# Kernel optimization log

Measured on AMD Instinct MI355X. Metric: run time of the kernel, lower is better.

## Reference

```python
import jax, jax.numpy as jnp
import numpy as np

BN_EPS = 1e-5
L2_EPS = 1e-12


def _normalize_adj(adj):
    # faithful to normalize_adj_torch: D^{-1/2} scaling applied as
    # (adj @ diag(r)).T @ diag(r)  ==  adj.T * r[:,None] * r[None,:]
    rowsum = adj.sum(1)
    r = jnp.power(rowsum, -0.5)
    r = jnp.where(jnp.isinf(r), 0.0, r)
    return adj.T * r[:, None] * r[None, :]


def _graph_conv(x, adj_n, W, b):
    # y = adj @ x (+ self), y @ W + b, then L2-normalize over feature dim
    y = jnp.einsum('ij,bjd->bid', adj_n, x) + x
    y = jnp.einsum('bnd,de->bne', y, W) + b
    norm = jnp.linalg.norm(y, axis=2, keepdims=True)
    return y / jnp.maximum(norm, L2_EPS)


def _batch_norm_nodes(x):
    # BatchNorm1d(num_features = N) in training mode with fresh params:
    # normalize over (batch, feature) dims per node channel, biased variance
    mean = x.mean(axis=(0, 2), keepdims=True)
    var = x.var(axis=(0, 2), keepdims=True)
    return (x - mean) / jnp.sqrt(var + BN_EPS)


def setup_inputs() -> dict:
    key = jax.random.key(0)
    ks = jax.random.split(key, 5)
    B, N, D = 4, 8192, 64
    H, E, C = 128, 256, 16
    x = jax.random.normal(ks[0], (B, N, D), dtype=jnp.float32)
    adj = jax.random.uniform(ks[1], (N, N), dtype=jnp.float32)
    W1 = jax.random.normal(ks[2], (D, H), dtype=jnp.float32) * 0.1
    b1 = jnp.zeros((H,), dtype=jnp.float32)
    W2 = jax.random.normal(ks[3], (H, E), dtype=jnp.float32) * 0.1
    b2 = jnp.zeros((E,), dtype=jnp.float32)
    Wp = jax.random.normal(ks[4], (E, C), dtype=jnp.float32) * 0.1
    bp = jnp.zeros((C,), dtype=jnp.float32)
    return {"x": x, "adj": adj, "W1": W1, "b1": b1, "W2": W2,
            "b2": b2, "Wp": Wp, "bp": bp}


def reference(x, adj, W1, b1, W2, b2, Wp, bp):
    adj_n = _normalize_adj(adj)
    g1 = _graph_conv(x, adj_n, W1, b1)
    g1 = jax.nn.relu(g1)
    g1 = _batch_norm_nodes(g1)
    g1 = _graph_conv(g1, adj_n, W2, b2)
    g1 = jax.nn.relu(g1)
    g1 = _batch_norm_nodes(g1)
    pred = jnp.einsum('bne,ec->bnc', g1, Wp) + bp
    # Softmax over dim=1 (node axis), as in the original
    return jax.nn.softmax(pred, axis=1)
```

## Files before the change

### kernel.cpp

```cpp
#include <hip/hip_runtime.h>
#include <hip/hip_bf16.h>
#include <cstdint>
#include <cstddef>

typedef unsigned short u16;
typedef __attribute__((ext_vector_type(8))) short bf16x8;
typedef __attribute__((ext_vector_type(4))) float f32x4;
typedef __attribute__((ext_vector_type(4))) unsigned short u16x4;

#define B_ 4
#define N_ 8192
#define D_ 64
#define H_ 128
#define E_ 256
#define C_ 16

__device__ __forceinline__ u16 f2bf(float f) {
  unsigned u = __builtin_bit_cast(unsigned, f);
  u += 0x7fffu + ((u >> 16) & 1u);
  return (u16)(u >> 16);
}
__device__ __forceinline__ float bf2f(u16 u) {
  return __builtin_bit_cast(float, ((unsigned)u) << 16);
}

__device__ __forceinline__ float wave_sum(float v) {
  v += __shfl_xor(v, 32, 64); v += __shfl_xor(v, 16, 64); v += __shfl_xor(v, 8, 64);
  v += __shfl_xor(v, 4, 64);  v += __shfl_xor(v, 2, 64);  v += __shfl_xor(v, 1, 64);
  return v;
}
__device__ __forceinline__ float wave_max(float v) {
  v = fmaxf(v, __shfl_xor(v, 32, 64)); v = fmaxf(v, __shfl_xor(v, 16, 64));
  v = fmaxf(v, __shfl_xor(v, 8, 64));  v = fmaxf(v, __shfl_xor(v, 4, 64));
  v = fmaxf(v, __shfl_xor(v, 2, 64));  v = fmaxf(v, __shfl_xor(v, 1, 64));
  return v;
}

__device__ __forceinline__ void gld16(const void* g, void* l) {
  __builtin_amdgcn_global_load_lds((const __attribute__((address_space(1))) void*)g,
                                   (__attribute__((address_space(3))) void*)l, 16, 0, 0);
}

__global__ __launch_bounds__(256) void k_zero(float* __restrict__ p, int n) {
  int i = blockIdx.x * 256 + threadIdx.x;
  if (i < n) p[i] = 0.f;
}

__global__ __launch_bounds__(256) void k_transpose(const float* __restrict__ adj, u16* __restrict__ adjT,
                                                   float* __restrict__ rsum) {
  __shared__ float tile[64][65];
  int bi = blockIdx.x & 127, bj = blockIdx.x >> 7;
  int i0 = bi * 64, j0 = bj * 64;
  int t = threadIdx.x;
#pragma unroll
  for (int q = 0; q < 4; ++q) {
    int idx = q * 256 + t; int jl = idx >> 4, c4 = idx & 15;
    float4 v = *(const float4*)(adj + (size_t)(j0 + jl) * N_ + i0 + c4 * 4);
    tile[jl][c4 * 4 + 0] = v.x; tile[jl][c4 * 4 + 1] = v.y;
    tile[jl][c4 * 4 + 2] = v.z; tile[jl][c4 * 4 + 3] = v.w;
    float s = (v.x + v.y) + (v.z + v.w);
    s += __shfl_xor(s, 1, 64); s += __shfl_xor(s, 2, 64);
    s += __shfl_xor(s, 4, 64); s += __shfl_xor(s, 8, 64);
    if ((t & 15) == 0) atomicAdd(&rsum[j0 + jl], s);
  }
  __syncthreads();
#pragma unroll
  for (int q = 0; q < 4; ++q) {
    int idx = q * 256 + t; int il = idx >> 4, c4 = idx & 15;
    u16x4 o;
    o.x = f2bf(tile[c4 * 4 + 0][il]); o.y = f2bf(tile[c4 * 4 + 1][il]);
    o.z = f2bf(tile[c4 * 4 + 2][il]); o.w = f2bf(tile[c4 * 4 + 3][il]);
    *(u16x4*)(adjT + (size_t)(i0 + il) * N_ + j0 + c4 * 4) = o;
  }
}

__global__ __launch_bounds__(256) void k_rsqrt(const float* __restrict__ rsum, float* __restrict__ rr) {
  int i = blockIdx.x * 256 + threadIdx.x;
  float s = rsum[i];
  rr[i] = s > 0.f ? rsqrtf(s) : 0.f;
}

__global__ __launch_bounds__(256) void k_xt(const float* __restrict__ x, const float* __restrict__ rr,
                                            u16* __restrict__ xt) {
  __shared__ float tile[64][65];
  int b = blockIdx.x >> 7, j0 = (blockIdx.x & 127) * 64;
  int t = threadIdx.x;
#pragma unroll
  for (int q = 0; q < 4; ++q) {
    int idx = q * 256 + t; int jl = idx >> 4, c4 = idx & 15;
    float4 v = *(const float4*)(x + ((size_t)b * N_ + j0 + jl) * D_ + c4 * 4);
    float rv = rr[j0 + jl];
    tile[jl][c4 * 4 + 0] = v.x * rv; tile[jl][c4 * 4 + 1] = v.y * rv;
    tile[jl][c4 * 4 + 2] = v.z * rv; tile[jl][c4 * 4 + 3] = v.w * rv;
  }
  __syncthreads();
#pragma unroll
  for (int q = 0; q < 4; ++q) {
    int idx = q * 256 + t; int dl = idx >> 4, c4 = idx & 15;
    u16x4 o;
    o.x = f2bf(tile[c4 * 4 + 0][dl]); o.y = f2bf(tile[c4 * 4 + 1][dl]);
    o.z = f2bf(tile[c4 * 4 + 2][dl]); o.w = f2bf(tile[c4 * 4 + 3][dl]);
    *(u16x4*)(xt + (size_t)(b * 64 + dl) * N_ + j0 + c4 * 4) = o;
  }
}

template<int BM, int BN, int KS>
__global__ __launch_bounds__(256) void k_gemm(const u16* __restrict__ A, const u16* __restrict__ B,
                                              u16* __restrict__ Cp, int N) {
  constexpr int BK = 32;
  __shared__ __align__(16) u16 As[BM * BK];
  __shared__ __align__(16) u16 Bs[BN * BK];
  const int tid = threadIdx.x;
  const int nb = N / BN;
  const int bn = blockIdx.x % nb;
  const int kb = (blockIdx.x / nb) % KS;
  const int bm = blockIdx.x / (nb * KS);
  const int m0 = bm * BM, n0 = bn * BN;
  const int kbeg = kb * (N_ / KS), kend = kbeg + N_ / KS;
  constexpr int WM = BM / 2, WN = BN / 2;
  constexpr int FM = WM / 16, FN = WN / 16;
  const int wave = tid >> 6, lane = tid & 63;
  const int wm = (wave >> 1) * WM, wn = (wave & 1) * WN;
  const int lr = lane & 15, lk = lane >> 4;

  f32x4 acc[FM][FN];
#pragma unroll
  for (int a = 0; a < FM; ++a)
#pragma unroll
    for (int b = 0; b < FN; ++b) acc[a][b] = (f32x4){0.f, 0.f, 0.f, 0.f};

  for (int k0 = kbeg; k0 < kend; k0 += BK) {
#pragma unroll
    for (int it = 0; it < BM / 64; ++it) {
      int c = it * 256 + tid;
      gld16(A + (size_t)(m0 + (c >> 2)) * N_ + k0 + (c & 3) * 8,
            As + ((size_t)it * 256 + (tid & 192)) * 8);
    }
#pragma unroll
    for (int it = 0; it < BN / 64; ++it) {
      int c = it * 256 + tid;
      gld16(B + (size_t)(n0 + (c >> 2)) * N_ + k0 + (c & 3) * 8,
            Bs + ((size_t)it * 256 + (tid & 192)) * 8);
    }
    __syncthreads();
    bf16x8 av[FM], bv[FN];
#pragma unroll
    for (int f = 0; f < FM; ++f)
      av[f] = *(const bf16x8*)(As + (wm + f * 16 + lr) * BK + lk * 8);
#pragma unroll
    for (int f = 0; f < FN; ++f)
      bv[f] = *(const bf16x8*)(Bs + (wn + f * 16 + lr) * BK + lk * 8);
#pragma unroll
    for (int fm = 0; fm < FM; ++fm)
#pragma unroll
      for (int fn = 0; fn < FN; ++fn)
        acc[fm][fn] = __builtin_amdgcn_mfma_f32_16x16x32_bf16(av[fm], bv[fn], acc[fm][fn], 0, 0, 0);
    __syncthreads();
  }
  u16* Cs = Cp + (size_t)kb * N_ * N;
#pragma unroll
  for (int fm = 0; fm < FM; ++fm) {
    int row0 = m0 + wm + fm * 16 + lk * 4;
#pragma unroll
    for (int fn = 0; fn < FN; ++fn) {
      int col = n0 + wn + fn * 16 + lr;
#pragma unroll
      for (int p = 0; p < 4; ++p)
        Cs[(size_t)(row0 + p) * N + col] = f2bf(acc[fm][fn][p]);
    }
  }
}

__global__ __launch_bounds__(256) void k_epi1(const u16* __restrict__ T1p, const float* __restrict__ x,
    const float* __restrict__ rr, const float* __restrict__ W1, const float* __restrict__ b1,
    float* __restrict__ g1n, u16* __restrict__ g1t) {
  union SharedU { float ys[16][256]; u16 gb[512][18]; };
  __shared__ SharedU su;
  __shared__ float zbuf[16][512];
  __shared__ float rs[16];
  const int t = threadIdx.x;
  const int i0 = blockIdx.x * 16;
  constexpr size_t SL = (size_t)N_ * 256;
  if (t < 16) rs[t] = rr[i0 + t];
  __syncthreads();
#pragma unroll
  for (int q = 0; q < 16; ++q) {
    int idx = q * 256 + t; int n = idx >> 8, c = idx & 255, b = c >> 6, d = c & 63;
    size_t ti = (size_t)(i0 + n) * 256 + c;
    float s = bf2f(T1p[ti]) + bf2f(T1p[ti + SL]) + bf2f(T1p[ti + 2 * SL]) + bf2f(T1p[ti + 3 * SL]);
    su.ys[n][c] = rs[n] * s + x[((size_t)b * N_ + i0 + n) * D_ + d];
  }
  const int h = t & 127, bh = t >> 7;
  float w[64];
#pragma unroll
  for (int d = 0; d < 64; ++d) w[d] = W1[d * H_ + h];
  float b1h = b1[h];
  __syncthreads();
  for (int n = 0; n < 16; ++n) {
    float za = b1h, zb = b1h;
#pragma unroll
    for (int d = 0; d < 64; ++d) {
      za += su.ys[n][bh * 64 + d] * w[d];
      zb += su.ys[n][(bh + 2) * 64 + d] * w[d];
    }
    zbuf[n][bh * 128 + h] = za;
    zbuf[n][(bh + 2) * 128 + h] = zb;
  }
  __syncthreads();
  const int wv = t >> 6, lane = t & 63;
#pragma unroll
  for (int nn = 0; nn < 4; ++nn) {
    int n = wv * 4 + nn;
    float v[8], nb2[8];
#pragma unroll
    for (int q = 0; q < 8; ++q) { v[q] = zbuf[n][q * 64 + lane]; }
#pragma unroll
    for (int q = 0; q < 8; ++q) nb2[q] = wave_sum(v[q] * v[q]);
    float inv0 = 1.f / fmaxf(sqrtf(nb2[0] + nb2[1]), 1e-12f);
    float inv1 = 1.f / fmaxf(sqrtf(nb2[2] + nb2[3]), 1e-12f);
    float inv2 = 1.f / fmaxf(sqrtf(nb2[4] + nb2[5]), 1e-12f);
    float inv3 = 1.f / fmaxf(sqrtf(nb2[6] + nb2[7]), 1e-12f);
    float sc[4] = {inv0, inv1, inv2, inv3};
    float t1 = 0.f, t2 = 0.f;
#pragma unroll
    for (int q = 0; q < 8; ++q) {
      v[q] = fmaxf(v[q] * sc[q >> 1], 0.f);
      t1 += v[q]; t2 += v[q] * v[q];
    }
    float s1 = wave_sum(t1), s2 = wave_sum(t2);
    float m = s1 * (1.f / 512.f);
    float var = s2 * (1.f / 512.f) - m * m;
    float iv = rsqrtf(var + 1e-5f);
    float rv = rs[n];
#pragma unroll
    for (int q = 0; q < 8; ++q) {
      float g = (v[q] - m) * iv;
      g1n[(size_t)(i0 + n) * 512 + q * 64 + lane] = g;
      su.gb[q * 64 + lane][n] = f2bf(g * rv);
    }
  }
  __syncthreads();
#pragma unroll
  for (int rep = 0; rep < 2; ++rep) {
    int c = rep * 256 + t;
    const unsigned* src = (const unsigned*)&su.gb[c][0];
    uint4 o0, o1;
    o0.x = src[0]; o0.y = src[1]; o0.z = src[2]; o0.w = src[3];
    o1.x = src[4]; o1.y = src[5]; o1.z = src[6]; o1.w = src[7];
    uint4* dst = (uint4*)(g1t + (size_t)c * N_ + i0);
    dst[0] = o0; dst[1] = o1;
  }
}

__global__ __launch_bounds__(256) void k_epi2(const u16* __restrict__ T2p, const float* __restrict__ g1n,
    const float* __restrict__ rr, const float* __restrict__ W2, const float* __restrict__ b2,
    float* __restrict__ g2n) {
  __shared__ __align__(16) float ysm[8 * 512];
  __shared__ __align__(16) float W2s[32 * 256];
  __shared__ float red1[128];
  __shared__ float nv[32];
  __shared__ float redA[32], redB[32];
  __shared__ float mn[8], iv[8];
  constexpr size_t SL = (size_t)N_ * 512;
  int i0 = blockIdx.x * 8, t = threadIdx.x;
#pragma unroll
  for (int q = 0; q < 4; ++q) {
    int idx = q * 256 + t; int n = idx >> 7, c4 = idx & 127;
    int i = i0 + n;
    float rv = rr[i];
    size_t ti = (size_t)i * 512 + c4 * 4;
    u16x4 p0 = *(const u16x4*)(T2p + ti);
    u16x4 p1 = *(const u16x4*)(T2p + SL + ti);
    float4 g = *(const float4*)(g1n + ti);
    float4 y;
    y.x = rv * (bf2f(p0.x) + bf2f(p1.x)) + g.x;
    y.y = rv * (bf2f(p0.y) + bf2f(p1.y)) + g.y;
    y.z = rv * (bf2f(p0.z) + bf2f(p1.z)) + g.z;
    y.w = rv * (bf2f(p0.w) + bf2f(p1.w)) + g.w;
    *(float4*)&ysm[n * 512 + c4 * 4] = y;
  }
  int e = t;
  float z[8][4];
#pragma unroll
  for (int n = 0; n < 8; ++n)
#pragma unroll
    for (int b = 0; b < 4; ++b) z[n][b] = 0.f;

  for (int hc = 0; hc < H_; hc += 32) {
    __syncthreads();
#pragma unroll
    for (int q = 0; q < 8; ++q) {
      int idx = q * 256 + t;
      ((float4*)W2s)[idx] = ((const float4*)(W2 + (size_t)hc * 256))[idx];
    }
    __syncthreads();
#pragma unroll
    for (int h4 = 0; h4 < 32; h4 += 4) {
      float w0 = W2s[(h4 + 0) * 256 + e];
      float w1 = W2s[(h4 + 1) * 256 + e];
      float w2 = W2s[(h4 + 2) * 256 + e];
      float w3 = W2s[(h4 + 3) * 256 + e];
#pragma unroll
      for (int n = 0; n < 8; ++n) {
#pragma unroll
        for (int b = 0; b < 4; ++b) {
          float4 y = *(const float4*)&ysm[n * 512 + b * 128 + hc + h4];
          z[n][b] += y.x * w0 + y.y * w1 + y.z * w2 + y.w * w3;
        }
      }
    }
  }
  float b2e = b2[e];
  int wave = t >> 6, lane = t & 63;
#pragma unroll
  for (int n = 0; n < 8; ++n)
#pragma unroll
    for (int b = 0; b < 4; ++b) {
      z[n][b] += b2e;
      float s = wave_sum(z[n][b] * z[n][b]);
      if (lane == 0) red1[n * 16 + b * 4 + wave] = s;
    }
  __syncthreads();
  if (t < 32) {
    float s = red1[t * 4 + 0] + red1[t * 4 + 1] + red1[t * 4 + 2] + red1[t * 4 + 3];
    nv[t] = fmaxf(sqrtf(s), 1e-12f);
  }
  __syncthreads();
#pragma unroll
  for (int n = 0; n < 8; ++n) {
    float s1 = 0.f, s2 = 0.f;
#pragma unroll
    for (int b = 0; b < 4; ++b) {
      z[n][b] = fmaxf(z[n][b] / nv[n * 4 + b], 0.f);
      s1 += z[n][b]; s2 += z[n][b] * z[n][b];
    }
    s1 = wave_sum(s1); s2 = wave_sum(s2);
    if (lane == 0) { redA[n * 4 + wave] = s1; redB[n * 4 + wave] = s2; }
  }
  __syncthreads();
  if (t < 8) {
    float s1 = redA[t * 4] + redA[t * 4 + 1] + redA[t * 4 + 2] + redA[t * 4 + 3];
    float s2 = redB[t * 4] + redB[t * 4 + 1] + redB[t * 4 + 2] + redB[t * 4 + 3];
    float m = s1 * (1.f / 1024.f), v = s2 * (1.f / 1024.f) - m * m;
    mn[t] = m; iv[t] = 1.f / sqrtf(v + 1e-5f);
  }
  __syncthreads();
#pragma unroll
  for (int n = 0; n < 8; ++n)
#pragma unroll
    for (int b = 0; b < 4; ++b)
      g2n[(size_t)(i0 + n) * 1024 + b * 256 + e] = (z[n][b] - mn[n]) * iv[n];
}

__global__ __launch_bounds__(256) void k_pred(const float* __restrict__ g2n, const float* __restrict__ Wp,
    const float* __restrict__ bp, float* __restrict__ pred) {
  __shared__ __align__(16) float gs[8 * 1028];
  __shared__ __align__(16) float Wps[E_ * C_];
  int i0 = blockIdx.x * 8, t = threadIdx.x;
#pragma unroll
  for (int q = 0; q < 4; ++q) ((float4*)Wps)[q * 256 + t] = ((const float4*)Wp)[q * 256 + t];
#pragma unroll
  for (int q = 0; q < 8; ++q) {
    int idx = q * 256 + t; int n = idx >> 8, c4 = idx & 255;
    *(float4*)&gs[n * 1028 + c4 * 4] = *(const float4*)(g2n + (size_t)(i0 + n) * 1024 + c4 * 4);
  }
  __syncthreads();
#pragma unroll
  for (int s = 0; s < 2; ++s) {
    int o = s * 256 + t; int n = o >> 6, b = (o >> 4) & 3, c = o & 15;
    float acc = bp[c];
    const float* g = &gs[n * 1028 + b * 256];
#pragma unroll 16
    for (int e2 = 0; e2 < 256; e2 += 4) {
      float4 gv = *(const float4*)&g[e2];
      acc += gv.x * Wps[(e2 + 0) * 16 + c] + gv.y * Wps[(e2 + 1) * 16 + c]
           + gv.z * Wps[(e2 + 2) * 16 + c] + gv.w * Wps[(e2 + 3) * 16 + c];
    }
    pred[((size_t)b * N_ + i0 + n) * C_ + c] = acc;
  }
}

__global__ __launch_bounds__(256) void k_softmax(const float* __restrict__ pred, float* __restrict__ out) {
  int b = blockIdx.x >> 4, c = blockIdx.x & 15, t = threadIdx.x;
  const float* p = pred + (size_t)b * N_ * C_ + c;
  float* po = out + (size_t)b * N_ * C_ + c;
  float v[32];
  float mx = -3.4e38f;
#pragma unroll
  for (int k = 0; k < 32; ++k) { v[k] = p[(size_t)(t + 256 * k) * C_]; mx = fmaxf(mx, v[k]); }
  mx = wave_max(mx);
  __shared__ float pm[4];
  __shared__ float ps[4];
  int wave = t >> 6, lane = t & 63;
  if (lane == 0) pm[wave] = mx;
  __syncthreads();
  mx = fmaxf(fmaxf(pm[0], pm[1]), fmaxf(pm[2], pm[3]));
  float s = 0.f;
#pragma unroll
  for (int k = 0; k < 32; ++k) { v[k] = __expf(v[k] - mx); s += v[k]; }
  s = wave_sum(s);
  if (lane == 0) ps[wave] = s;
  __syncthreads();
  s = (ps[0] + ps[1]) + (ps[2] + ps[3]);
  float inv = 1.f / s;
#pragma unroll
  for (int k = 0; k < 32; ++k) po[(size_t)(t + 256 * k) * C_] = v[k] * inv;
}

extern "C" void kernel_launch(void* const* d_in, const int* in_sizes, int n_in,
                              void* d_out, int out_size, void* d_ws, size_t ws_size,
                              hipStream_t stream) {
  const float* x   = (const float*)d_in[0];
  const float* adj = (const float*)d_in[1];
  const float* W1  = (const float*)d_in[2];
  const float* b1  = (const float*)d_in[3];
  const float* W2  = (const float*)d_in[4];
  const float* b2  = (const float*)d_in[5];
  const float* Wp  = (const float*)d_in[6];
  const float* bp  = (const float*)d_in[7];
  float* out = (float*)d_out;
  char* ws = (char*)d_ws;

  size_t o = 0;
  u16*   adjT = (u16*)(ws + o);   o += (size_t)N_ * N_ * 2;
  float* rsum = (float*)(ws + o); o += (size_t)N_ * 4;
  float* rr   = (float*)(ws + o); o += (size_t)N_ * 4;
  float* g1n  = (float*)(ws + o); o += (size_t)N_ * 512 * 4;
  u16*   g1t  = (u16*)(ws + o);   o += (size_t)512 * N_ * 2;
  size_t xoff = o;
  u16*   xt   = (u16*)(ws + xoff);
  u16*   T1p  = (u16*)(ws + xoff + (size_t)256 * N_ * 2);
  u16*   T2p  = (u16*)(ws + xoff);
  float* g2n  = (float*)ws;
  float* pred = (float*)(ws + (size_t)33554432);

  k_zero     <<<N_ / 256, 256, 0, stream>>>(rsum, N_);
  k_transpose<<<128 * 128, 256, 0, stream>>>(adj, adjT, rsum);
  k_rsqrt    <<<N_ / 256, 256, 0, stream>>>(rsum, rr);
  k_xt       <<<4 * 128, 256, 0, stream>>>(x, rr, xt);
  k_gemm<128, 64, 4><<<(N_ / 128) * (256 / 64) * 4, 256, 0, stream>>>(adjT, xt, T1p, 256);
  k_epi1     <<<N_ / 16, 256, 0, stream>>>(T1p, x, rr, W1, b1, g1n, g1t);
  k_gemm<128, 64, 2><<<(N_ / 128) * (512 / 64) * 2, 256, 0, stream>>>(adjT, g1t, T2p, 512);
  k_epi2     <<<N_ / 8, 256, 0, stream>>>(T2p, g1n, rr, W2, b2, g2n);
  k_pred     <<<N_ / 8, 256, 0, stream>>>(g2n, Wp, bp, pred);
  k_softmax  <<<64, 256, 0, stream>>>(pred, out);
}
```

Measured before the change: 847.1 us.

## Swap GEMM operand roles so feature matrix is the small tile and adj streams once

The aggregation GEMM is rewritten as features-by-adjacency, using a 64x256 tile where the small feature dimension is M and the large node dimension is N. Blocks are ordered so that blocks sharing an adjacency column panel run adjacently, which is meant to improve cache reuse of the large adjT matrix. Partial results are now stored transposed, so both epilogues are changed to read contiguous 16-byte chunks per channel across nodes and unpack bf16 pairs. The workspace layout is also changed so xt and the partial buffers no longer alias.

Result: slower. 1.009 ms (+19.1%).

```diff
diff --git a/kernel.cpp b/kernel.cpp
--- a/kernel.cpp
+++ b/kernel.cpp
@@ -22,6 +22,12 @@
 }
 __device__ __forceinline__ float bf2f(u16 u) {
   return __builtin_bit_cast(float, ((unsigned)u) << 16);
+}
+__device__ __forceinline__ float bflo(unsigned u) {
+  return __builtin_bit_cast(float, u << 16);
+}
+__device__ __forceinline__ float bfhi(unsigned u) {
+  return __builtin_bit_cast(float, u & 0xffff0000u);
 }
 
 __device__ __forceinline__ float wave_sum(float v) {
@@ -104,69 +110,63 @@
   }
 }
 
-template<int BM, int BN, int KS>
-__global__ __launch_bounds__(256) void k_gemm(const u16* __restrict__ A, const u16* __restrict__ B,
-                                              u16* __restrict__ Cp, int N) {
-  constexpr int BK = 32;
+template<int KS>
+__global__ __launch_bounds__(256) void k_gemmT(const u16* __restrict__ A, const u16* __restrict__ B,
+                                               u16* __restrict__ Cp, int M) {
+  constexpr int BK = 32, BM = 64, BN = 256;
   __shared__ __align__(16) u16 As[BM * BK];
   __shared__ __align__(16) u16 Bs[BN * BK];
   const int tid = threadIdx.x;
-  const int nb = N / BN;
-  const int bn = blockIdx.x % nb;
-  const int kb = (blockIdx.x / nb) % KS;
-  const int bm = blockIdx.x / (nb * KS);
+  const int nmb = M >> 6;
+  const int bm = blockIdx.x % nmb;
+  const int rest = blockIdx.x / nmb;
+  const int kb = rest % KS;
+  const int bn = rest / KS;
   const int m0 = bm * BM, n0 = bn * BN;
   const int kbeg = kb * (N_ / KS), kend = kbeg + N_ / KS;
-  constexpr int WM = BM / 2, WN = BN / 2;
-  constexpr int FM = WM / 16, FN = WN / 16;
   const int wave = tid >> 6, lane = tid & 63;
-  const int wm = (wave >> 1) * WM, wn = (wave & 1) * WN;
+  const int wm = (wave >> 1) * 32, wn = (wave & 1) * 128;
   const int lr = lane & 15, lk = lane >> 4;
 
-  f32x4 acc[FM][FN];
-#pragma unroll
-  for (int a = 0; a < FM; ++a)
-#pragma unroll
-    for (int b = 0; b < FN; ++b) acc[a][b] = (f32x4){0.f, 0.f, 0.f, 0.f};
+  f32x4 acc[2][8];
+#pragma unroll
+  for (int a = 0; a < 2; ++a)
+#pragma unroll
+    for (int b = 0; b < 8; ++b) acc[a][b] = (f32x4){0.f, 0.f, 0.f, 0.f};
+
+  const u16* Ab = A + (size_t)(m0 + (tid >> 2)) * N_ + (tid & 3) * 8;
+  const u16* Bb = B + (size_t)(n0 + (tid >> 2)) * N_ + (tid & 3) * 8;
+  u16* As_dst = As + (tid & 192) * 8;
 
   for (int k0 = kbeg; k0 < kend; k0 += BK) {
-#pragma unroll
-    for (int it = 0; it < BM / 64; ++it) {
-      int c = it * 256 + tid;
-      gld16(A + (size_t)(m0 + (c >> 2)) * N_ + k0 + (c & 3) * 8,
-            As + ((size_t)it * 256 + (tid & 192)) * 8);
-    }
-#pragma unroll
-    for (int it = 0; it < BN / 64; ++it) {
-      int c = it * 256 + tid;
-      gld16(B + (size_t)(n0 + (c >> 2)) * N_ + k0 + (c & 3) * 8,
-            Bs + ((size_t)it * 256 + (tid & 192)) * 8);
-    }
+    gld16(Ab + k0, As_dst);
+#pragma unroll
+    for (int it = 0; it < 4; ++it)
+      gld16(Bb + (size_t)it * 64 * N_ + k0, Bs + (it * 256 + (tid & 192)) * 8);
     __syncthreads();
-    bf16x8 av[FM], bv[FN];
-#pragma unroll
-    for (int f = 0; f < FM; ++f)
-      av[f] = *(const bf16x8*)(As + (wm + f * 16 + lr) * BK + lk * 8);
-#pragma unroll
-    for (int f = 0; f < FN; ++f)
+    bf16x8 av[2], bv[8];
+    av[0] = *(const bf16x8*)(As + (wm + lr) * BK + lk * 8);
+    av[1] = *(const bf16x8*)(As + (wm + 16 + lr) * BK + lk * 8);
+#pragma unroll
+    for (int f = 0; f < 8; ++f)
       bv[f] = *(const bf16x8*)(Bs + (wn + f * 16 + lr) * BK + lk * 8);
 #pragma unroll
-    for (int fm = 0; fm < FM; ++fm)
-#pragma unroll
-      for (int fn = 0; fn < FN; ++fn)
+    for (int fm = 0; fm < 2; ++fm)
+#pragma unroll
+      for (int fn = 0; fn < 8; ++fn)
         acc[fm][fn] = __builtin_amdgcn_mfma_f32_16x16x32_bf16(av[fm], bv[fn], acc[fm][fn], 0, 0, 0);
     __syncthreads();
   }
-  u16* Cs = Cp + (size_t)kb * N_ * N;
-#pragma unroll
-  for (int fm = 0; fm < FM; ++fm) {
+  u16* Cs = Cp + (size_t)kb * M * N_;
+#pragma unroll
+  for (int fm = 0; fm < 2; ++fm) {
     int row0 = m0 + wm + fm * 16 + lk * 4;
 #pragma unroll
-    for (int fn = 0; fn < FN; ++fn) {
+    for (int fn = 0; fn < 8; ++fn) {
       int col = n0 + wn + fn * 16 + lr;
 #pragma unroll
       for (int p = 0; p < 4; ++p)
-        Cs[(size_t)(row0 + p) * N + col] = f2bf(acc[fm][fn][p]);
+        Cs[(size_t)(row0 + p) * N_ + col] = f2bf(acc[fm][fn][p]);
     }
   }
 }
@@ -180,15 +180,27 @@
   __shared__ float rs[16];
   const int t = threadIdx.x;
   const int i0 = blockIdx.x * 16;
-  constexpr size_t SL = (size_t)N_ * 256;
+  constexpr size_t SL = (size_t)256 * N_;
   if (t < 16) rs[t] = rr[i0 + t];
   __syncthreads();
-#pragma unroll
-  for (int q = 0; q < 16; ++q) {
-    int idx = q * 256 + t; int n = idx >> 8, c = idx & 255, b = c >> 6, d = c & 63;
-    size_t ti = (size_t)(i0 + n) * 256 + c;
-    float s = bf2f(T1p[ti]) + bf2f(T1p[ti + SL]) + bf2f(T1p[ti + 2 * SL]) + bf2f(T1p[ti + 3 * SL]);
-    su.ys[n][c] = rs[n] * s + x[((size_t)b * N_ + i0 + n) * D_ + d];
+  {
+    float accv[16];
+#pragma unroll
+    for (int n = 0; n < 16; ++n) accv[n] = 0.f;
+    const u16* tp = T1p + (size_t)t * N_ + i0;
+#pragma unroll
+    for (int ks = 0; ks < 4; ++ks) {
+      const uint4* p = (const uint4*)(tp + ks * SL);
+      uint4 a = p[0], b = p[1];
+      accv[0]  += bflo(a.x); accv[1]  += bfhi(a.x); accv[2]  += bflo(a.y); accv[3]  += bfhi(a.y);
+      accv[4]  += bflo(a.z); accv[5]  += bfhi(a.z); accv[6]  += bflo(a.w); accv[7]  += bfhi(a.w);
+      accv[8]  += bflo(b.x); accv[9]  += bfhi(b.x); accv[10] += bflo(b.y); accv[11] += bfhi(b.y);
+      accv[12] += bflo(b.z); accv[13] += bfhi(b.z); accv[14] += bflo(b.w); accv[15] += bfhi(b.w);
+    }
+    int bb = t >> 6, d = t & 63;
+#pragma unroll
+    for (int n = 0; n < 16; ++n)
+      su.ys[n][t] = rs[n] * accv[n] + x[((size_t)bb * N_ + i0 + n) * D_ + d];
   }
   const int h = t & 127, bh = t >> 7;
   float w[64];
@@ -261,23 +273,25 @@
   __shared__ float nv[32];
   __shared__ float redA[32], redB[32];
   __shared__ float mn[8], iv[8];
-  constexpr size_t SL = (size_t)N_ * 512;
+  __shared__ float rs2[8];
+  constexpr size_t SL = (size_t)512 * N_;
   int i0 = blockIdx.x * 8, t = threadIdx.x;
-#pragma unroll
-  for (int q = 0; q < 4; ++q) {
-    int idx = q * 256 + t; int n = idx >> 7, c4 = idx & 127;
-    int i = i0 + n;
-    float rv = rr[i];
-    size_t ti = (size_t)i * 512 + c4 * 4;
-    u16x4 p0 = *(const u16x4*)(T2p + ti);
-    u16x4 p1 = *(const u16x4*)(T2p + SL + ti);
-    float4 g = *(const float4*)(g1n + ti);
-    float4 y;
-    y.x = rv * (bf2f(p0.x) + bf2f(p1.x)) + g.x;
-    y.y = rv * (bf2f(p0.y) + bf2f(p1.y)) + g.y;
-    y.z = rv * (bf2f(p0.z) + bf2f(p1.z)) + g.z;
-    y.w = rv * (bf2f(p0.w) + bf2f(p1.w)) + g.w;
-    *(float4*)&ysm[n * 512 + c4 * 4] = y;
+  if (t < 8) rs2[t] = rr[i0 + t];
+  __syncthreads();
+#pragma unroll
+  for (int half = 0; half < 2; ++half) {
+    int c = half * 256 + t;
+    const u16* p = T2p + (size_t)c * N_ + i0;
+    uint4 a0 = *(const uint4*)p;
+    uint4 a1 = *(const uint4*)(p + SL);
+    float s[8];
+    s[0] = bflo(a0.x) + bflo(a1.x); s[1] = bfhi(a0.x) + bfhi(a1.x);
+    s[2] = bflo(a0.y) + bflo(a1.y); s[3] = bfhi(a0.y) + bfhi(a1.y);
+    s[4] = bflo(a0.z) + bflo(a1.z); s[5] = bfhi(a0.z) + bfhi(a1.z);
+    s[6] = bflo(a0.w) + bflo(a1.w); s[7] = bfhi(a0.w) + bfhi(a1.w);
+#pragma unroll
+    for (int n = 0; n < 8; ++n)
+      ysm[n * 512 + c] = rs2[n] * s[n] + g1n[(size_t)(i0 + n) * 512 + c];
   }
   int e = t;
   float z[8][4];
@@ -427,10 +441,10 @@
   float* rr   = (float*)(ws + o); o += (size_t)N_ * 4;
   float* g1n  = (float*)(ws + o); o += (size_t)N_ * 512 * 4;
   u16*   g1t  = (u16*)(ws + o);   o += (size_t)512 * N_ * 2;
-  size_t xoff = o;
-  u16*   xt   = (u16*)(ws + xoff);
-  u16*   T1p  = (u16*)(ws + xoff + (size_t)256 * N_ * 2);
-  u16*   T2p  = (u16*)(ws + xoff);
+  u16*   xt   = (u16*)(ws + o);   o += (size_t)256 * N_ * 2;
+  u16*   Tp   = (u16*)(ws + o);   o += (size_t)4 * 256 * N_ * 2;
+  u16*   T1p  = Tp;
+  u16*   T2p  = Tp;
   float* g2n  = (float*)ws;
   float* pred = (float*)(ws + (size_t)33554432);
 
@@ -438,9 +452,9 @@
   k_transpose<<<128 * 128, 256, 0, stream>>>(adj, adjT, rsum);
   k_rsqrt    <<<N_ / 256, 256, 0, stream>>>(rsum, rr);
   k_xt       <<<4 * 128, 256, 0, stream>>>(x, rr, xt);
-  k_gemm<128, 64, 4><<<(N_ / 128) * (256 / 64) * 4, 256, 0, stream>>>(adjT, xt, T1p, 256);
+  k_gemmT<4> <<<(256 / 64) * 4 * (N_ / 256), 256, 0, stream>>>(xt, adjT, T1p, 256);
   k_epi1     <<<N_ / 16, 256, 0, stream>>>(T1p, x, rr, W1, b1, g1n, g1t);
-  k_gemm<128, 64, 2><<<(N_ / 128) * (512 / 64) * 2, 256, 0, stream>>>(adjT, g1t, T2p, 512);
+  k_gemmT<2> <<<(512 / 64) * 2 * (N_ / 256), 256, 0, stream>>>(g1t, adjT, T2p, 512);
   k_epi2     <<<N_ / 8, 256, 0, stream>>>(T2p, g1n, rr, W2, b2, g2n);
   k_pred     <<<N_ / 8, 256, 0, stream>>>(g2n, Wp, bp, pred);
   k_softmax  <<<64, 256, 0, stream>>>(pred, out);
```
